# Optimization experiments

Hardware: AMD Instinct MI355X
Metric: run time of the kernel (lower is better)

The kernel has to match this reference:

```python
import jax, jax.numpy as jnp
import numpy as np
from jax.scipy.linalg import expm

S = 64          # alphabet size (codons)
M = 8           # number of models, prod(model_shape)
N_LEAVES = 32   # leaves of the balanced binary tree
N_EDGES = 62    # nodes 0..62, every non-root node has one parent edge (edge id == child node id)
B = 1024        # batch (alignment columns)
# per-level ranges of child-node ids; node 32+j has children (2j, 2j+1), etc.
LEVELS = [(0, 32), (32, 48), (48, 56), (56, 60), (60, 62)]


def inv_stereographic_projection(p):
    # maps R^{s-1} -> unit sphere S^{s-1}
    n2 = jnp.sum(p * p, axis=-1, keepdims=True)
    return jnp.concatenate([2.0 * p / (n2 + 1.0), (n2 - 1.0) / (n2 + 1.0)], axis=-1)


def generator(R, pi):
    # R: (M, s(s-1)/2) exchangeabilities, pi: (M, s) stationary distribution
    iu, ju = np.triu_indices(S, 1)
    A = jnp.zeros((M, S, S), R.dtype).at[:, iu, ju].set(R).at[:, ju, iu].set(R)
    Q = A * pi[:, None, :]                       # Q_ij = A_ij * pi_j (off-diagonal)
    row = jnp.sum(Q, axis=-1)                    # (M, S)
    return Q - jnp.eye(S, dtype=Q.dtype) * row[:, :, None]


def felsenstein(leave_configuration, R_inv, pi_inv, lengths):
    pi = inv_stereographic_projection(pi_inv) ** 2           # (M, S), rows sum to 1
    R = jnp.exp(R_inv)                                       # positive rates
    Q = generator(R, pi)                                     # (M, S, S)
    tQ = lengths[:, None, None, None] * Q[None]              # (E, M, S, S)
    P = jax.vmap(expm)(tQ.reshape(-1, S, S)).reshape(N_EDGES, M, S, S)
    # leaf alphas: tile leaf observations over the M models -> (n_leaves, B, M, S)
    prev = jnp.broadcast_to(
        leave_configuration.transpose(1, 0, 2)[:, :, None, :],
        (N_LEAVES, leave_configuration.shape[0], M, S))
    # level-synchronous pruning: messages up each parent edge, then product of the two children
    for a, b in LEVELS:
        msg = jnp.einsum('emcd,ebmd->ebmc', P[a:b], prev)    # per-edge transition
        prev = msg[0::2] * msg[1::2]                         # combine sibling pairs
    root = prev[0]                                           # (B, M, S)
    out = jnp.einsum('bms,ms->bm', root, pi)                 # P(data | model m)
    return out.reshape(out.shape[0], M)                      # (B, *model_shape)


def setup_inputs() -> dict:
    key = jax.random.key(0)
    k1, k2, k3, k4 = jax.random.split(key, 4)
    leave_configuration = jax.random.uniform(k1, (B, N_LEAVES, S), dtype=jnp.float32)
    tree_indices = jnp.zeros((B,), dtype=jnp.int32)          # single tree (F=1)
    R_inv = jax.random.uniform(k2, (M, S * (S - 1) // 2), dtype=jnp.float32,
                               minval=-1.0, maxval=1.0)
    pi_inv = jnp.full((M, S - 1), 1.0 / (np.sqrt(S) - 1.0), dtype=jnp.float32) \
        + 0.01 * jax.random.normal(k3, (M, S - 1), dtype=jnp.float32)
    lengths = jax.random.uniform(k4, (N_EDGES,), dtype=jnp.float32,
                                 minval=0.05, maxval=0.5)
    return {'leave_configuration': leave_configuration, 'R_inv': R_inv,
            'pi_inv': pi_inv, 'lengths': lengths, 'tree_indices': tree_indices}


def reference(leave_configuration, R_inv, pi_inv, lengths, tree_indices):
    # F=1: tf.dynamic_partition/gather_nd batch slicing is the identity, so
    # tree_indices is closed over / unused.
    return felsenstein(leave_configuration, R_inv, pi_inv, lengths)
```

## Files before the change

### kernel.cpp

```cpp
#include <hip/hip_runtime.h>

typedef unsigned short u16;
typedef unsigned int u32;
typedef __attribute__((ext_vector_type(8))) __bf16 bf16x8;
typedef __attribute__((ext_vector_type(4))) float f32x4;

constexpr size_t OFF_PI  = 0;
constexpr size_t OFF_PBH = 512;
constexpr size_t OFF_PBL = OFF_PBH + 1015808;

union FR { uint4 u; bf16x8 v; };

__device__ __forceinline__ void split_bf16(float x, u16& h, u16& l) {
  u32 b = __float_as_uint(x);
  u32 hb = (b + 0x7fffu + ((b >> 16) & 1u)) & 0xffff0000u;
  h = (u16)(hb >> 16);
  float r = x - __uint_as_float(hb);
  l = (u16)(__float_as_uint(r) >> 16);
}

__device__ __forceinline__ void split8(const f32x4 a, const f32x4 b,
                                       uint4& hi, uint4& lo) {
  u16 h[8], l[8];
  split_bf16(a.x, h[0], l[0]); split_bf16(a.y, h[1], l[1]);
  split_bf16(a.z, h[2], l[2]); split_bf16(a.w, h[3], l[3]);
  split_bf16(b.x, h[4], l[4]); split_bf16(b.y, h[5], l[5]);
  split_bf16(b.z, h[6], l[6]); split_bf16(b.w, h[7], l[7]);
  hi.x = h[0] | ((u32)h[1] << 16); hi.y = h[2] | ((u32)h[3] << 16);
  hi.z = h[4] | ((u32)h[5] << 16); hi.w = h[6] | ((u32)h[7] << 16);
  lo.x = l[0] | ((u32)l[1] << 16); lo.y = l[2] | ((u32)l[3] << 16);
  lo.z = l[4] | ((u32)l[5] << 16); lo.w = l[6] | ((u32)l[7] << 16);
}

__device__ __forceinline__ void mfma3(f32x4& a, const uint4 ah, const uint4 al,
                                      const uint4 bh, const uint4 bl) {
  FR Ah, Al, Bh, Bl;
  Ah.u = ah; Al.u = al; Bh.u = bh; Bl.u = bl;
  a = __builtin_amdgcn_mfma_f32_16x16x32_bf16(Ah.v, Bh.v, a, 0, 0, 0);
  a = __builtin_amdgcn_mfma_f32_16x16x32_bf16(Ah.v, Bl.v, a, 0, 0, 0);
  a = __builtin_amdgcn_mfma_f32_16x16x32_bf16(Al.v, Bh.v, a, 0, 0, 0);
}

__device__ __forceinline__ void xt_read2(const u32* b, int row, int chunk,
                                         uint4& hi, uint4& lo) {
  const int dw = (row << 5) + (((chunk + row) & 7) << 2);
  hi = *(const uint4*)&b[dw];
  lo = *(const uint4*)&b[2048 + dw];
}
__device__ __forceinline__ void xt_write4(u32* b, int row, int cp, int half,
                                          const f32x4 v) {
  u16 h[4], l[4];
  split_bf16(v.x, h[0], l[0]); split_bf16(v.y, h[1], l[1]);
  split_bf16(v.z, h[2], l[2]); split_bf16(v.w, h[3], l[3]);
  const int dw = (row << 5) + (((cp + row) & 7) << 2) + half * 2;
  uint2 hh, ll;
  hh.x = h[0] | ((u32)h[1] << 16); hh.y = h[2] | ((u32)h[3] << 16);
  ll.x = l[0] | ((u32)l[1] << 16); ll.y = l[2] | ((u32)l[3] << 16);
  *(uint2*)&b[dw] = hh;
  *(uint2*)&b[2048 + dw] = ll;
}

__global__ __launch_bounds__(512, 2) void k_pcomb(
    const float* __restrict__ R_inv, const float* __restrict__ pi_inv,
    const float* __restrict__ lengths, float* __restrict__ ws,
    u16* __restrict__ PBH, u16* __restrict__ PBL) {
  const int m = blockIdx.x & 7, prt = blockIdx.x >> 3;
  const int tid = threadIdx.x, lane = tid & 63, w = tid >> 6;
  const int ln = lane & 15, kq = lane >> 4;
  __shared__ float pis[64];
  __shared__ float n2s;
  __shared__ __align__(16) float Qs[64 * 68];
  __shared__ __align__(16) u32 PB[8][4096];

  if (tid < 64) {
    float p = (tid < 63) ? pi_inv[m * 63 + tid] : 0.f;
    float v = p * p;
    #pragma unroll
    for (int off = 32; off; off >>= 1) v += __shfl_down(v, off, 64);
    if (tid == 0) n2s = v;
  }
  __syncthreads();
  if (tid < 64) {
    const float den = n2s + 1.f;
    const float x = (tid < 63) ? 2.f * pi_inv[m * 63 + tid] / den
                               : (n2s - 1.f) / den;
    const float pv = x * x;
    pis[tid] = pv;
    if (prt == 0) ws[OFF_PI + (size_t)m * 64 + tid] = pv;
  }
  __syncthreads();
  for (int idx = tid; idx < 4096; idx += 512) {
    const int i = idx >> 6, j = idx & 63;
    float q = 0.f;
    if (i != j) {
      const int a = min(i, j), b = max(i, j);
      const int kk = a * (127 - a) / 2 + (b - a - 1);
      q = expf(R_inv[m * 2016 + kk]) * pis[j];
    }
    Qs[i * 68 + j] = q;
  }
  __syncthreads();
  if (tid < 64) {
    float s = 0.f;
    #pragma unroll 4
    for (int j4 = 0; j4 < 64; j4 += 4) {
      const f32x4 q = *(const f32x4*)&Qs[tid * 68 + j4];
      s += q.x + q.y + q.z + q.w;
    }
    Qs[tid * 68 + tid] = -s;
  }
  __syncthreads();
  float q[12][8];
  #pragma unroll
  for (int g = 0; g < 2; ++g) {
    const int vt = tid + 512 * g;
    const int ci0 = vt >> 4, cj0 = (vt & 15) * 4;
    #pragma unroll
    for (int r = 0; r < 4; ++r) q[0][g * 4 + r] = Qs[ci0 * 68 + cj0 + r];
  }
  {
    const int i = tid >> 3, c = tid & 7;
    const f32x4 a = *(const f32x4*)&Qs[i * 68 + c * 8];
    const f32x4 b = *(const f32x4*)&Qs[i * 68 + c * 8 + 4];
    uint4 h, l;
    split8(a, b, h, l);
    const int dw = (i << 5) + (((c + i) & 7) << 2);
    *(uint4*)&PB[0][dw] = h;
    *(uint4*)&PB[0][2048 + dw] = l;
    const int j = i;
    f32x4 ca, cb;
    ca.x = Qs[(c * 8 + 0) * 68 + j]; ca.y = Qs[(c * 8 + 1) * 68 + j];
    ca.z = Qs[(c * 8 + 2) * 68 + j]; ca.w = Qs[(c * 8 + 3) * 68 + j];
    cb.x = Qs[(c * 8 + 4) * 68 + j]; cb.y = Qs[(c * 8 + 5) * 68 + j];
    cb.z = Qs[(c * 8 + 6) * 68 + j]; cb.w = Qs[(c * 8 + 7) * 68 + j];
    split8(ca, cb, h, l);
    *(uint4*)&PB[4][dw] = h;
    *(uint4*)&PB[4][2048 + dw] = l;
  }
  __syncthreads();

  const f32x4 z = {0.f, 0.f, 0.f, 0.f};
  auto mm = [&](const u32* RX, const u32* CY, u32* dstC, u32* dstR) {
    #pragma unroll
    for (int tt = 0; tt < 2; ++tt) {
      const int T = w + tt * 8;
      const int ct = T >> 2, bt = T & 3;
      uint4 ah[2], al[2], bh[2], bl[2];
      #pragma unroll
      for (int kh = 0; kh < 2; ++kh) {
        xt_read2(RX, ct * 16 + ln, kh * 4 + kq, ah[kh], al[kh]);
        xt_read2(CY, bt * 16 + ln, kh * 4 + kq, bh[kh], bl[kh]);
      }
      f32x4 a = z;
      #pragma unroll
      for (int kh = 0; kh < 2; ++kh) mfma3(a, ah[kh], al[kh], bh[kh], bl[kh]);
      #pragma unroll
      for (int r = 0; r < 4; ++r)
        Qs[(ct * 16 + kq * 4 + r) * 64 + bt * 16 + ln] = a[r];
      if (dstC) xt_write4(dstC, bt * 16 + ln, 2 * ct + (kq >> 1), kq & 1, a);
      if (dstR) {
        uint4 ch[2], cl[2], dh[2], dl[2];
        #pragma unroll
        for (int kh = 0; kh < 2; ++kh) {
          xt_read2(CY, ct * 16 + ln, kh * 4 + kq, ch[kh], cl[kh]);
          xt_read2(RX, bt * 16 + ln, kh * 4 + kq, dh[kh], dl[kh]);
        }
        f32x4 a2 = z;
        #pragma unroll
        for (int kh = 0; kh < 2; ++kh) mfma3(a2, ch[kh], cl[kh], dh[kh], dl[kh]);
        xt_write4(dstR, bt * 16 + ln, 2 * ct + (kq >> 1), kq & 1, a2);
      }
    }
  };
  auto step = [&](const u32* RX, const u32* CY, int k, u32* dstC, u32* dstR) {
    mm(RX, CY, dstC, dstR);
    __syncthreads();
    #pragma unroll
    for (int g = 0; g < 2; ++g) {
      const int vt = tid + 512 * g;
      #pragma unroll
      for (int r = 0; r < 4; ++r) q[k - 1][g * 4 + r] = Qs[vt * 4 + r];
    }
    __syncthreads();
  };
  step(PB[0], PB[4], 2, PB[5], PB[1]);
  step(PB[1], PB[4], 3, PB[6], nullptr);
  step(PB[1], PB[5], 4, PB[7], PB[2]);
  step(PB[2], PB[4], 5, nullptr, nullptr);
  step(PB[2], PB[5], 6, nullptr, nullptr);
  step(PB[2], PB[6], 7, nullptr, nullptr);
  step(PB[2], PB[7], 8, nullptr, PB[3]);
  step(PB[3], PB[4], 9, nullptr, nullptr);
  step(PB[3], PB[5], 10, nullptr, nullptr);
  step(PB[3], PB[6], 11, nullptr, nullptr);
  step(PB[3], PB[7], 12, nullptr, nullptr);

  #pragma unroll
  for (int ei = 0; ei < 2; ++ei) {
    const int e = prt * 2 + ei;
    if (e >= 62) break;
    const float t = lengths[e];
    float av[8] = {0.f, 0.f, 0.f, 0.f, 0.f, 0.f, 0.f, 0.f};
    #pragma unroll
    for (int g = 0; g < 2; ++g) {
      const int vt = tid + 512 * g;
      const int dr = (vt >> 4) - ((vt & 15) * 4);
      if (dr >= 0 && dr < 4) av[g * 4 + dr] = 1.f;
    }
    float cf = 1.f;
    #pragma unroll
    for (int k = 1; k <= 12; ++k) {
      cf *= t / (float)k;
      #pragma unroll
      for (int r = 0; r < 8; ++r) av[r] = fmaf(cf, q[k - 1][r], av[r]);
    }
    #pragma unroll
    for (int g = 0; g < 2; ++g) {
      const int vt = tid + 512 * g;
      u16 h[4], l[4];
      split_bf16(av[g * 4 + 0], h[0], l[0]);
      split_bf16(av[g * 4 + 1], h[1], l[1]);
      split_bf16(av[g * 4 + 2], h[2], l[2]);
      split_bf16(av[g * 4 + 3], h[3], l[3]);
      const size_t base = (((size_t)e * 8 + m) << 12) + (size_t)vt * 4;
      ushort4 h4, l4;
      h4.x = h[0]; h4.y = h[1]; h4.z = h[2]; h4.w = h[3];
      l4.x = l[0]; l4.y = l[1]; l4.z = l[2]; l4.w = l[3];
      *(ushort4*)(PBH + base) = h4;
      *(ushort4*)(PBL + base) = l4;
    }
  }
}

__global__ __launch_bounds__(512, 2) void k_tree(
    const float* __restrict__ leaves, const u16* __restrict__ Phi,
    const u16* __restrict__ Plo, const float* __restrict__ ws,
    float* __restrict__ out) {
  const int m = blockIdx.x & 7, btile = blockIdx.x >> 3;
  const int tid = threadIdx.x, lane = tid & 63, w = tid >> 6;
  const int ln = lane & 15, kq = lane >> 4;
  __shared__ __align__(16) u32 slots[16 * 2048];
  __shared__ float psum[2][4][16];
  const f32x4 z = {0.f, 0.f, 0.f, 0.f};

  auto node_read = [&](int slot, int row, int kh, uint4& bh, uint4& bl) {
    const int jc = kh * 8 + kq * 2;
    const u32* b = &slots[slot * 2048 + row * 64];
    const uint4 A = *(const uint4*)&b[((jc + row) & 15) << 2];
    const uint4 B = *(const uint4*)&b[((jc + 1 + row) & 15) << 2];
    bh.x = A.x; bh.y = A.y; bh.z = B.x; bh.w = B.y;
    bl.x = A.z; bl.y = A.w; bl.z = B.z; bl.w = B.w;
  };
  auto node_write = [&](int slot, int row, int jc, const f32x4 v) {
    u16 h[4], l[4];
    split_bf16(v.x, h[0], l[0]); split_bf16(v.y, h[1], l[1]);
    split_bf16(v.z, h[2], l[2]); split_bf16(v.w, h[3], l[3]);
    uint4 pk;
    pk.x = h[0] | ((u32)h[1] << 16); pk.y = h[2] | ((u32)h[3] << 16);
    pk.z = l[0] | ((u32)l[1] << 16); pk.w = l[2] | ((u32)l[3] << 16);
    *(uint4*)&slots[slot * 2048 + row * 64 + (((jc + row) & 15) << 2)] = pk;
  };

  auto do_pair = [&](int eb, int p, int s0, int s1, int outSlot, int bt0,
                     int nbt, int ct0, int nct, bool leaf, f32x4* rootout) {
    uint4 bfh[2][2][2], bfl[2][2][2];
    #pragma unroll
    for (int s = 0; s < 2; ++s)
      #pragma unroll
      for (int bi = 0; bi < 2; ++bi) {
        if (bi >= nbt) continue;
        const int row = (bt0 + bi) * 16 + ln;
        #pragma unroll
        for (int kh = 0; kh < 2; ++kh) {
          if (leaf) {
            const float* g = leaves + (size_t)(btile * 32 + row) * 2048 +
                             (size_t)(eb + 2 * p + s) * 64 + kh * 32 + kq * 8;
            const f32x4 xa = *(const f32x4*)g;
            const f32x4 xb = *(const f32x4*)(g + 4);
            split8(xa, xb, bfh[s][bi][kh], bfl[s][bi][kh]);
          } else {
            node_read(s ? s1 : s0, row, kh, bfh[s][bi][kh], bfl[s][bi][kh]);
          }
        }
      }
    uint4 ph[2][4][2], pl[2][4][2];
    #pragma unroll
    for (int s = 0; s < 2; ++s) {
      const size_t pb = ((size_t)(eb + 2 * p + s) * 8 + m) << 12;
      #pragma unroll
      for (int ci = 0; ci < 4; ++ci) {
        if (ci >= nct) continue;
        #pragma unroll
        for (int kh = 0; kh < 2; ++kh) {
          const size_t off =
              pb + (size_t)((ct0 + ci) * 16 + ln) * 64 + kh * 32 + kq * 8;
          ph[s][ci][kh] = *(const uint4*)(Phi + off);
          pl[s][ci][kh] = *(const uint4*)(Plo + off);
        }
      }
    }
    f32x4 a0[4][2];
    #pragma unroll
    for (int ci = 0; ci < 4; ++ci) {
      if (ci >= nct) continue;
      #pragma unroll
      for (int bi = 0; bi < 2; ++bi) {
        if (bi >= nbt) continue;
        f32x4 a = z;
        #pragma unroll
        for (int kh = 0; kh < 2; ++kh)
          mfma3(a, ph[0][ci][kh], pl[0][ci][kh], bfh[0][bi][kh], bfl[0][bi][kh]);
        a0[ci][bi] = a;
      }
    }
    #pragma unroll
    for (int ci = 0; ci < 4; ++ci) {
      if (ci >= nct) continue;
      #pragma unroll
      for (int bi = 0; bi < 2; ++bi) {
        if (bi >= nbt) continue;
        f32x4 a = z;
        #pragma unroll
        for (int kh = 0; kh < 2; ++kh)
          mfma3(a, ph[1][ci][kh], pl[1][ci][kh], bfh[1][bi][kh], bfl[1][bi][kh]);
        const f32x4 pr = a0[ci][bi] * a;
        if (rootout)
          *rootout = pr;
        else
          node_write(outSlot, (bt0 + bi) * 16 + ln, (ct0 + ci) * 4 + kq, pr);
      }
    }
  };

  do_pair(0, w, -1, -1, w, 0, 2, 0, 4, true, nullptr);
  do_pair(0, w + 8, -1, -1, w + 8, 0, 2, 0, 4, true, nullptr);
  __syncthreads();
  do_pair(32, w, 2 * w, 2 * w + 1, 2 * w, 0, 2, 0, 4, false, nullptr);
  __syncthreads();
  {
    const int j = w >> 1, bi = w & 1;
    do_pair(48, j, 4 * j, 4 * j + 2, 4 * j, bi, 1, 0, 4, false, nullptr);
  }
  __syncthreads();
  {
    const int j = w >> 2, bi = w & 1, ch = (w >> 1) & 1;
    do_pair(56, j, 8 * j, 8 * j + 4, 8 * j + 1, bi, 1, ch * 2, 2, false,
            nullptr);
  }
  __syncthreads();
  {
    f32x4 pr = z;
    do_pair(60, 0, 1, 9, -1, w & 1, 1, w >> 1, 1, false, &pr);
    const f32x4 piv =
        *(const f32x4*)&ws[OFF_PI + (size_t)m * 64 + (w >> 1) * 16 + kq * 4];
    float v = pr.x * piv.x + pr.y * piv.y + pr.z * piv.z + pr.w * piv.w;
    v += __shfl_xor(v, 16, 64);
    v += __shfl_xor(v, 32, 64);
    if (lane < 16) psum[w & 1][w >> 1][lane] = v;
  }
  __syncthreads();
  if (tid < 32) {
    const int bi = tid >> 4, bb = tid & 15;
    out[(size_t)(btile * 32 + tid) * 8 + m] =
        psum[bi][0][bb] + psum[bi][1][bb] + psum[bi][2][bb] + psum[bi][3][bb];
  }
}

extern "C" void kernel_launch(void* const* d_in, const int* in_sizes, int n_in,
                              void* d_out, int out_size, void* d_ws, size_t ws_size,
                              hipStream_t stream) {
  const float* leaves  = (const float*)d_in[0];
  const float* R_inv   = (const float*)d_in[1];
  const float* pi_inv  = (const float*)d_in[2];
  const float* lengths = (const float*)d_in[3];
  float* out = (float*)d_out;
  float* ws  = (float*)d_ws;

  u16* PBH = (u16*)(ws + OFF_PBH);
  u16* PBL = (u16*)(ws + OFF_PBL);

  hipLaunchKernelGGL(k_pcomb, dim3(256), dim3(512), 0, stream, R_inv, pi_inv,
                     lengths, ws, PBH, PBL);
  hipLaunchKernelGGL(k_tree, dim3(256), dim3(512), 0, stream, leaves, PBH, PBL,
                     ws, out);
}
```

Measured before the change: 122.5 us.

## Fuse P-matrix build and tree pruning into one kernel with a grid barrier

Merges the transition-matrix build kernel and the tree-pruning kernel into a single launch of 256 blocks. An atomic-counter grid-wide barrier separates the two phases, and both phases share one shared-memory buffer. The aim is to remove the second launch and the inter-kernel gap. The barrier assumes all 256 blocks are co-resident, otherwise it deadlocks, and the 2-blocks-per-CU launch bound was dropped.

```diff
diff --git a/kernel.cpp b/kernel.cpp
--- a/kernel.cpp
+++ b/kernel.cpp
@@ -10,6 +10,8 @@
 constexpr size_t OFF_PBL = OFF_PBH + 1015808;
 
 union FR { uint4 u; bf16x8 v; };
+
+__device__ unsigned g_bar = 0;
 
 __device__ __forceinline__ void split_bf16(float x, u16& h, u16& l) {
   u32 b = __float_as_uint(x);
@@ -60,309 +62,328 @@
   *(uint2*)&b[2048 + dw] = ll;
 }
 
-__global__ __launch_bounds__(512, 2) void k_pcomb(
-    const float* __restrict__ R_inv, const float* __restrict__ pi_inv,
-    const float* __restrict__ lengths, float* __restrict__ ws,
-    u16* __restrict__ PBH, u16* __restrict__ PBL) {
-  const int m = blockIdx.x & 7, prt = blockIdx.x >> 3;
+__global__ __launch_bounds__(512) void k_fused(
+    const float* __restrict__ leaves, const float* __restrict__ R_inv,
+    const float* __restrict__ pi_inv, const float* __restrict__ lengths,
+    float* __restrict__ ws, u16* __restrict__ PBH, u16* __restrict__ PBL,
+    float* __restrict__ out) {
+  const int m = blockIdx.x & 7;
   const int tid = threadIdx.x, lane = tid & 63, w = tid >> 6;
   const int ln = lane & 15, kq = lane >> 4;
-  __shared__ float pis[64];
-  __shared__ float n2s;
-  __shared__ __align__(16) float Qs[64 * 68];
-  __shared__ __align__(16) u32 PB[8][4096];
-
-  if (tid < 64) {
-    float p = (tid < 63) ? pi_inv[m * 63 + tid] : 0.f;
-    float v = p * p;
-    #pragma unroll
-    for (int off = 32; off; off >>= 1) v += __shfl_down(v, off, 64);
-    if (tid == 0) n2s = v;
-  }
-  __syncthreads();
-  if (tid < 64) {
-    const float den = n2s + 1.f;
-    const float x = (tid < 63) ? 2.f * pi_inv[m * 63 + tid] / den
-                               : (n2s - 1.f) / den;
-    const float pv = x * x;
-    pis[tid] = pv;
-    if (prt == 0) ws[OFF_PI + (size_t)m * 64 + tid] = pv;
-  }
-  __syncthreads();
-  for (int idx = tid; idx < 4096; idx += 512) {
-    const int i = idx >> 6, j = idx & 63;
-    float q = 0.f;
-    if (i != j) {
-      const int a = min(i, j), b = max(i, j);
-      const int kk = a * (127 - a) / 2 + (b - a - 1);
-      q = expf(R_inv[m * 2016 + kk]) * pis[j];
-    }
-    Qs[i * 68 + j] = q;
-  }
-  __syncthreads();
-  if (tid < 64) {
-    float s = 0.f;
-    #pragma unroll 4
-    for (int j4 = 0; j4 < 64; j4 += 4) {
-      const f32x4 q = *(const f32x4*)&Qs[tid * 68 + j4];
-      s += q.x + q.y + q.z + q.w;
-    }
-    Qs[tid * 68 + tid] = -s;
-  }
-  __syncthreads();
-  float q[12][8];
-  #pragma unroll
-  for (int g = 0; g < 2; ++g) {
-    const int vt = tid + 512 * g;
-    const int ci0 = vt >> 4, cj0 = (vt & 15) * 4;
-    #pragma unroll
-    for (int r = 0; r < 4; ++r) q[0][g * 4 + r] = Qs[ci0 * 68 + cj0 + r];
-  }
+  __shared__ __align__(16) u32 smem[37200];
+  const f32x4 z = {0.f, 0.f, 0.f, 0.f};
+
   {
-    const int i = tid >> 3, c = tid & 7;
-    const f32x4 a = *(const f32x4*)&Qs[i * 68 + c * 8];
-    const f32x4 b = *(const f32x4*)&Qs[i * 68 + c * 8 + 4];
-    uint4 h, l;
-    split8(a, b, h, l);
-    const int dw = (i << 5) + (((c + i) & 7) << 2);
-    *(uint4*)&PB[0][dw] = h;
-    *(uint4*)&PB[0][2048 + dw] = l;
-    const int j = i;
-    f32x4 ca, cb;
-    ca.x = Qs[(c * 8 + 0) * 68 + j]; ca.y = Qs[(c * 8 + 1) * 68 + j];
-    ca.z = Qs[(c * 8 + 2) * 68 + j]; ca.w = Qs[(c * 8 + 3) * 68 + j];
-    cb.x = Qs[(c * 8 + 4) * 68 + j]; cb.y = Qs[(c * 8 + 5) * 68 + j];
-    cb.z = Qs[(c * 8 + 6) * 68 + j]; cb.w = Qs[(c * 8 + 7) * 68 + j];
-    split8(ca, cb, h, l);
-    *(uint4*)&PB[4][dw] = h;
-    *(uint4*)&PB[4][2048 + dw] = l;
-  }
-  __syncthreads();
-
-  const f32x4 z = {0.f, 0.f, 0.f, 0.f};
-  auto mm = [&](const u32* RX, const u32* CY, u32* dstC, u32* dstR) {
-    #pragma unroll
-    for (int tt = 0; tt < 2; ++tt) {
-      const int T = w + tt * 8;
-      const int ct = T >> 2, bt = T & 3;
-      uint4 ah[2], al[2], bh[2], bl[2];
-      #pragma unroll
-      for (int kh = 0; kh < 2; ++kh) {
-        xt_read2(RX, ct * 16 + ln, kh * 4 + kq, ah[kh], al[kh]);
-        xt_read2(CY, bt * 16 + ln, kh * 4 + kq, bh[kh], bl[kh]);
-      }
-      f32x4 a = z;
-      #pragma unroll
-      for (int kh = 0; kh < 2; ++kh) mfma3(a, ah[kh], al[kh], bh[kh], bl[kh]);
-      #pragma unroll
-      for (int r = 0; r < 4; ++r)
-        Qs[(ct * 16 + kq * 4 + r) * 64 + bt * 16 + ln] = a[r];
-      if (dstC) xt_write4(dstC, bt * 16 + ln, 2 * ct + (kq >> 1), kq & 1, a);
-      if (dstR) {
-        uint4 ch[2], cl[2], dh[2], dl[2];
-        #pragma unroll
-        for (int kh = 0; kh < 2; ++kh) {
-          xt_read2(CY, ct * 16 + ln, kh * 4 + kq, ch[kh], cl[kh]);
-          xt_read2(RX, bt * 16 + ln, kh * 4 + kq, dh[kh], dl[kh]);
-        }
-        f32x4 a2 = z;
-        #pragma unroll
-        for (int kh = 0; kh < 2; ++kh) mfma3(a2, ch[kh], cl[kh], dh[kh], dl[kh]);
-        xt_write4(dstR, bt * 16 + ln, 2 * ct + (kq >> 1), kq & 1, a2);
-      }
-    }
-  };
-  auto step = [&](const u32* RX, const u32* CY, int k, u32* dstC, u32* dstR) {
-    mm(RX, CY, dstC, dstR);
-    __syncthreads();
+    const int prt = blockIdx.x >> 3;
+    float* pis = (float*)smem;
+    float* Qs  = (float*)&smem[80];
+    u32* PB    = &smem[4432];
+
+    if (tid < 64) {
+      float p = (tid < 63) ? pi_inv[m * 63 + tid] : 0.f;
+      float v = p * p;
+      #pragma unroll
+      for (int off = 32; off; off >>= 1) v += __shfl_down(v, off, 64);
+      if (tid == 0) ((float*)smem)[64] = v;
+    }
+    __syncthreads();
+    if (tid < 64) {
+      const float n2v = ((float*)smem)[64];
+      const float den = n2v + 1.f;
+      const float x = (tid < 63) ? 2.f * pi_inv[m * 63 + tid] / den
+                                 : (n2v - 1.f) / den;
+      const float pv = x * x;
+      pis[tid] = pv;
+      if (prt == 0) ws[OFF_PI + (size_t)m * 64 + tid] = pv;
+    }
+    __syncthreads();
+    for (int idx = tid; idx < 4096; idx += 512) {
+      const int i = idx >> 6, j = idx & 63;
+      float q = 0.f;
+      if (i != j) {
+        const int a = min(i, j), b = max(i, j);
+        const int kk = a * (127 - a) / 2 + (b - a - 1);
+        q = expf(R_inv[m * 2016 + kk]) * pis[j];
+      }
+      Qs[i * 68 + j] = q;
+    }
+    __syncthreads();
+    if (tid < 64) {
+      float s = 0.f;
+      #pragma unroll 4
+      for (int j4 = 0; j4 < 64; j4 += 4) {
+        const f32x4 q = *(const f32x4*)&Qs[tid * 68 + j4];
+        s += q.x + q.y + q.z + q.w;
+      }
+      Qs[tid * 68 + tid] = -s;
+    }
+    __syncthreads();
+    float q[12][8];
     #pragma unroll
     for (int g = 0; g < 2; ++g) {
       const int vt = tid + 512 * g;
-      #pragma unroll
-      for (int r = 0; r < 4; ++r) q[k - 1][g * 4 + r] = Qs[vt * 4 + r];
-    }
-    __syncthreads();
-  };
-  step(PB[0], PB[4], 2, PB[5], PB[1]);
-  step(PB[1], PB[4], 3, PB[6], nullptr);
-  step(PB[1], PB[5], 4, PB[7], PB[2]);
-  step(PB[2], PB[4], 5, nullptr, nullptr);
-  step(PB[2], PB[5], 6, nullptr, nullptr);
-  step(PB[2], PB[6], 7, nullptr, nullptr);
-  step(PB[2], PB[7], 8, nullptr, PB[3]);
-  step(PB[3], PB[4], 9, nullptr, nullptr);
-  step(PB[3], PB[5], 10, nullptr, nullptr);
-  step(PB[3], PB[6], 11, nullptr, nullptr);
-  step(PB[3], PB[7], 12, nullptr, nullptr);
-
-  #pragma unroll
-  for (int ei = 0; ei < 2; ++ei) {
-    const int e = prt * 2 + ei;
-    if (e >= 62) break;
-    const float t = lengths[e];
-    float av[8] = {0.f, 0.f, 0.f, 0.f, 0.f, 0.f, 0.f, 0.f};
+      const int ci0 = vt >> 4, cj0 = (vt & 15) * 4;
+      #pragma unroll
+      for (int r = 0; r < 4; ++r) q[0][g * 4 + r] = Qs[ci0 * 68 + cj0 + r];
+    }
+    {
+      const int i = tid >> 3, c = tid & 7;
+      const f32x4 a = *(const f32x4*)&Qs[i * 68 + c * 8];
+      const f32x4 b = *(const f32x4*)&Qs[i * 68 + c * 8 + 4];
+      uint4 h, l;
+      split8(a, b, h, l);
+      const int dw = (i << 5) + (((c + i) & 7) << 2);
+      *(uint4*)&PB[dw] = h;
+      *(uint4*)&PB[2048 + dw] = l;
+      const int j = i;
+      f32x4 ca, cb;
+      ca.x = Qs[(c * 8 + 0) * 68 + j]; ca.y = Qs[(c * 8 + 1) * 68 + j];
+      ca.z = Qs[(c * 8 + 2) * 68 + j]; ca.w = Qs[(c * 8 + 3) * 68 + j];
+      cb.x = Qs[(c * 8 + 4) * 68 + j]; cb.y = Qs[(c * 8 + 5) * 68 + j];
+      cb.z = Qs[(c * 8 + 6) * 68 + j]; cb.w = Qs[(c * 8 + 7) * 68 + j];
+      split8(ca, cb, h, l);
+      *(uint4*)&PB[4 * 4096 + dw] = h;
+      *(uint4*)&PB[4 * 4096 + 2048 + dw] = l;
+    }
+    __syncthreads();
+
+    auto mm = [&](const u32* RX, const u32* CY, u32* dstC, u32* dstR) {
+      #pragma unroll
+      for (int tt = 0; tt < 2; ++tt) {
+        const int T = w + tt * 8;
+        const int ct = T >> 2, bt = T & 3;
+        uint4 ah[2], al[2], bh[2], bl[2];
+        #pragma unroll
+        for (int kh = 0; kh < 2; ++kh) {
+          xt_read2(RX, ct * 16 + ln, kh * 4 + kq, ah[kh], al[kh]);
+          xt_read2(CY, bt * 16 + ln, kh * 4 + kq, bh[kh], bl[kh]);
+        }
+        f32x4 a = z;
+        #pragma unroll
+        for (int kh = 0; kh < 2; ++kh) mfma3(a, ah[kh], al[kh], bh[kh], bl[kh]);
+        #pragma unroll
+        for (int r = 0; r < 4; ++r)
+          Qs[(ct * 16 + kq * 4 + r) * 64 + bt * 16 + ln] = a[r];
+        if (dstC) xt_write4(dstC, bt * 16 + ln, 2 * ct + (kq >> 1), kq & 1, a);
+        if (dstR) {
+          uint4 ch[2], cl[2], dh[2], dl[2];
+          #pragma unroll
+          for (int kh = 0; kh < 2; ++kh) {
+            xt_read2(CY, ct * 16 + ln, kh * 4 + kq, ch[kh], cl[kh]);
+            xt_read2(RX, bt * 16 + ln, kh * 4 + kq, dh[kh], dl[kh]);
+          }
+          f32x4 a2 = z;
+          #pragma unroll
+          for (int kh = 0; kh < 2; ++kh)
+            mfma3(a2, ch[kh], cl[kh], dh[kh], dl[kh]);
+          xt_write4(dstR, bt * 16 + ln, 2 * ct + (kq >> 1), kq & 1, a2);
+        }
+      }
+    };
+    auto step = [&](const u32* RX, const u32* CY, int k, u32* dstC, u32* dstR) {
+      mm(RX, CY, dstC, dstR);
+      __syncthreads();
+      #pragma unroll
+      for (int g = 0; g < 2; ++g) {
+        const int vt = tid + 512 * g;
+        #pragma unroll
+        for (int r = 0; r < 4; ++r) q[k - 1][g * 4 + r] = Qs[vt * 4 + r];
+      }
+      __syncthreads();
+    };
+    u32* P0 = PB;            u32* P1 = PB + 1 * 4096;
+    u32* P2 = PB + 2 * 4096; u32* P3 = PB + 3 * 4096;
+    u32* P4 = PB + 4 * 4096; u32* P5 = PB + 5 * 4096;
+    u32* P6 = PB + 6 * 4096; u32* P7 = PB + 7 * 4096;
+    step(P0, P4, 2, P5, P1);
+    step(P1, P4, 3, P6, nullptr);
+    step(P1, P5, 4, P7, P2);
+    step(P2, P4, 5, nullptr, nullptr);
+    step(P2, P5, 6, nullptr, nullptr);
+    step(P2, P6, 7, nullptr, nullptr);
+    step(P2, P7, 8, nullptr, P3);
+    step(P3, P4, 9, nullptr, nullptr);
+    step(P3, P5, 10, nullptr, nullptr);
+    step(P3, P6, 11, nullptr, nullptr);
+    step(P3, P7, 12, nullptr, nullptr);
+
     #pragma unroll
-    for (int g = 0; g < 2; ++g) {
-      const int vt = tid + 512 * g;
-      const int dr = (vt >> 4) - ((vt & 15) * 4);
-      if (dr >= 0 && dr < 4) av[g * 4 + dr] = 1.f;
-    }
-    float cf = 1.f;
-    #pragma unroll
-    for (int k = 1; k <= 12; ++k) {
-      cf *= t / (float)k;
-      #pragma unroll
-      for (int r = 0; r < 8; ++r) av[r] = fmaf(cf, q[k - 1][r], av[r]);
-    }
-    #pragma unroll
-    for (int g = 0; g < 2; ++g) {
-      const int vt = tid + 512 * g;
+    for (int ei = 0; ei < 2; ++ei) {
+      const int e = prt * 2 + ei;
+      if (e >= 62) break;
+      const float t = lengths[e];
+      float av[8] = {0.f, 0.f, 0.f, 0.f, 0.f, 0.f, 0.f, 0.f};
+      #pragma unroll
+      for (int g = 0; g < 2; ++g) {
+        const int vt = tid + 512 * g;
+        const int dr = (vt >> 4) - ((vt & 15) * 4);
+        if (dr >= 0 && dr < 4) av[g * 4 + dr] = 1.f;
+      }
+      float cf = 1.f;
+      #pragma unroll
+      for (int k = 1; k <= 12; ++k) {
+        cf *= t / (float)k;
+        #pragma unroll
+        for (int r = 0; r < 8; ++r) av[r] = fmaf(cf, q[k - 1][r], av[r]);
+      }
+      #pragma unroll
+      for (int g = 0; g < 2; ++g) {
+        const int vt = tid + 512 * g;
+        u16 h[4], l[4];
+        split_bf16(av[g * 4 + 0], h[0], l[0]);
+        split_bf16(av[g * 4 + 1], h[1], l[1]);
+        split_bf16(av[g * 4 + 2], h[2], l[2]);
+        split_bf16(av[g * 4 + 3], h[3], l[3]);
+        const size_t base = (((size_t)e * 8 + m) << 12) + (size_t)vt * 4;
+        ushort4 h4, l4;
+        h4.x = h[0]; h4.y = h[1]; h4.z = h[2]; h4.w = h[3];
+        l4.x = l[0]; l4.y = l[1]; l4.z = l[2]; l4.w = l[3];
+        *(ushort4*)(PBH + base) = h4;
+        *(ushort4*)(PBL + base) = l4;
+      }
+    }
+  }
+
+  __syncthreads();
+  if (tid == 0) {
+    __threadfence();
+    const unsigned old = atomicAdd(&g_bar, 1u);
+    const unsigned target = (old & ~255u) + 256u;
+    while (__hip_atomic_load(&g_bar, __ATOMIC_ACQUIRE,
+                             __HIP_MEMORY_SCOPE_AGENT) < target)
+      __builtin_amdgcn_s_sleep(2);
+  }
+  __syncthreads();
+
+  {
+    const int btile = blockIdx.x >> 3;
+    u32* slots = smem;
+    float* psum = (float*)&smem[32768];
+
+    auto node_read = [&](int slot, int row, int kh, uint4& bh, uint4& bl) {
+      const int jc = kh * 8 + kq * 2;
+      const u32* b = &slots[slot * 2048 + row * 64];
+      const uint4 A = *(const uint4*)&b[((jc + row) & 15) << 2];
+      const uint4 B = *(const uint4*)&b[((jc + 1 + row) & 15) << 2];
+      bh.x = A.x; bh.y = A.y; bh.z = B.x; bh.w = B.y;
+      bl.x = A.z; bl.y = A.w; bl.z = B.z; bl.w = B.w;
+    };
+    auto node_write = [&](int slot, int row, int jc, const f32x4 v) {
       u16 h[4], l[4];
-      split_bf16(av[g * 4 + 0], h[0], l[0]);
-      split_bf16(av[g * 4 + 1], h[1], l[1]);
-      split_bf16(av[g * 4 + 2], h[2], l[2]);
-      split_bf16(av[g * 4 + 3], h[3], l[3]);
-      const size_t base = (((size_t)e * 8 + m) << 12) + (size_t)vt * 4;
-      ushort4 h4, l4;
-      h4.x = h[0]; h4.y = h[1]; h4.z = h[2]; h4.w = h[3];
-      l4.x = l[0]; l4.y = l[1]; l4.z = l[2]; l4.w = l[3];
-      *(ushort4*)(PBH + base) = h4;
-      *(ushort4*)(PBL + base) = l4;
-    }
-  }
-}
-
-__global__ __launch_bounds__(512, 2) void k_tree(
-    const float* __restrict__ leaves, const u16* __restrict__ Phi,
-    const u16* __restrict__ Plo, const float* __restrict__ ws,
-    float* __restrict__ out) {
-  const int m = blockIdx.x & 7, btile = blockIdx.x >> 3;
-  const int tid = threadIdx.x, lane = tid & 63, w = tid >> 6;
-  const int ln = lane & 15, kq = lane >> 4;
-  __shared__ __align__(16) u32 slots[16 * 2048];
-  __shared__ float psum[2][4][16];
-  const f32x4 z = {0.f, 0.f, 0.f, 0.f};
-
-  auto node_read = [&](int slot, int row, int kh, uint4& bh, uint4& bl) {
-    const int jc = kh * 8 + kq * 2;
-    const u32* b = &slots[slot * 2048 + row * 64];
-    const uint4 A = *(const uint4*)&b[((jc + row) & 15) << 2];
-    const uint4 B = *(const uint4*)&b[((jc + 1 + row) & 15) << 2];
-    bh.x = A.x; bh.y = A.y; bh.z = B.x; bh.w = B.y;
-    bl.x = A.z; bl.y = A.w; bl.z = B.z; bl.w = B.w;
-  };
-  auto node_write = [&](int slot, int row, int jc, const f32x4 v) {
-    u16 h[4], l[4];
-    split_bf16(v.x, h[0], l[0]); split_bf16(v.y, h[1], l[1]);
-    split_bf16(v.z, h[2], l[2]); split_bf16(v.w, h[3], l[3]);
-    uint4 pk;
-    pk.x = h[0] | ((u32)h[1] << 16); pk.y = h[2] | ((u32)h[3] << 16);
-    pk.z = l[0] | ((u32)l[1] << 16); pk.w = l[2] | ((u32)l[3] << 16);
-    *(uint4*)&slots[slot * 2048 + row * 64 + (((jc + row) & 15) << 2)] = pk;
-  };
-
-  auto do_pair = [&](int eb, int p, int s0, int s1, int outSlot, int bt0,
-                     int nbt, int ct0, int nct, bool leaf, f32x4* rootout) {
-    uint4 bfh[2][2][2], bfl[2][2][2];
-    #pragma unroll
-    for (int s = 0; s < 2; ++s)
-      #pragma unroll
-      for (int bi = 0; bi < 2; ++bi) {
-        if (bi >= nbt) continue;
-        const int row = (bt0 + bi) * 16 + ln;
-        #pragma unroll
-        for (int kh = 0; kh < 2; ++kh) {
-          if (leaf) {
-            const float* g = leaves + (size_t)(btile * 32 + row) * 2048 +
-                             (size_t)(eb + 2 * p + s) * 64 + kh * 32 + kq * 8;
-            const f32x4 xa = *(const f32x4*)g;
-            const f32x4 xb = *(const f32x4*)(g + 4);
-            split8(xa, xb, bfh[s][bi][kh], bfl[s][bi][kh]);
-          } else {
-            node_read(s ? s1 : s0, row, kh, bfh[s][bi][kh], bfl[s][bi][kh]);
+      split_bf16(v.x, h[0], l[0]); split_bf16(v.y, h[1], l[1]);
+      split_bf16(v.z, h[2], l[2]); split_bf16(v.w, h[3], l[3]);
+      uint4 pk;
+      pk.x = h[0] | ((u32)h[1] << 16); pk.y = h[2] | ((u32)h[3] << 16);
+      pk.z = l[0] | ((u32)l[1] << 16); pk.w = l[2] | ((u32)l[3] << 16);
+      *(uint4*)&slots[slot * 2048 + row * 64 + (((jc + row) & 15) << 2)] = pk;
+    };
+
+    auto do_pair = [&](int eb, int p, int s0, int s1, int outSlot, int bt0,
+                       int nbt, int ct0, int nct, bool leaf, f32x4* rootout) {
+      uint4 bfh[2][2][2], bfl[2][2][2];
+      #pragma unroll
+      for (int s = 0; s < 2; ++s)
+        #pragma unroll
+        for (int bi = 0; bi < 2; ++bi) {
+          if (bi >= nbt) continue;
+          const int row = (bt0 + bi) * 16 + ln;
+          #pragma unroll
+          for (int kh = 0; kh < 2; ++kh) {
+            if (leaf) {
+              const float* g = leaves + (size_t)(btile * 32 + row) * 2048 +
+                               (size_t)(eb + 2 * p + s) * 64 + kh * 32 + kq * 8;
+              const f32x4 xa = *(const f32x4*)g;
+              const f32x4 xb = *(const f32x4*)(g + 4);
+              split8(xa, xb, bfh[s][bi][kh], bfl[s][bi][kh]);
+            } else {
+              node_read(s ? s1 : s0, row, kh, bfh[s][bi][kh], bfl[s][bi][kh]);
+            }
           }
         }
-      }
-    uint4 ph[2][4][2], pl[2][4][2];
-    #pragma unroll
-    for (int s = 0; s < 2; ++s) {
-      const size_t pb = ((size_t)(eb + 2 * p + s) * 8 + m) << 12;
+      uint4 ph[2][4][2], pl[2][4][2];
+      #pragma unroll
+      for (int s = 0; s < 2; ++s) {
+        const size_t pb = ((size_t)(eb + 2 * p + s) * 8 + m) << 12;
+        #pragma unroll
+        for (int ci = 0; ci < 4; ++ci) {
+          if (ci >= nct) continue;
+          #pragma unroll
+          for (int kh = 0; kh < 2; ++kh) {
+            const size_t off =
+                pb + (size_t)((ct0 + ci) * 16 + ln) * 64 + kh * 32 + kq * 8;
+            ph[s][ci][kh] = *(const uint4*)(PBH + off);
+            pl[s][ci][kh] = *(const uint4*)(PBL + off);
+          }
+        }
+      }
+      f32x4 a0[4][2];
       #pragma unroll
       for (int ci = 0; ci < 4; ++ci) {
         if (ci >= nct) continue;
         #pragma unroll
-        for (int kh = 0; kh < 2; ++kh) {
-          const size_t off =
-              pb + (size_t)((ct0 + ci) * 16 + ln) * 64 + kh * 32 + kq * 8;
-          ph[s][ci][kh] = *(const uint4*)(Phi + off);
-          pl[s][ci][kh] = *(const uint4*)(Plo + off);
-        }
-      }
-    }
-    f32x4 a0[4][2];
-    #pragma unroll
-    for (int ci = 0; ci < 4; ++ci) {
-      if (ci >= nct) continue;
-      #pragma unroll
-      for (int bi = 0; bi < 2; ++bi) {
-        if (bi >= nbt) continue;
-        f32x4 a = z;
-        #pragma unroll
-        for (int kh = 0; kh < 2; ++kh)
-          mfma3(a, ph[0][ci][kh], pl[0][ci][kh], bfh[0][bi][kh], bfl[0][bi][kh]);
-        a0[ci][bi] = a;
-      }
-    }
-    #pragma unroll
-    for (int ci = 0; ci < 4; ++ci) {
-      if (ci >= nct) continue;
-      #pragma unroll
-      for (int bi = 0; bi < 2; ++bi) {
-        if (bi >= nbt) continue;
-        f32x4 a = z;
-        #pragma unroll
-        for (int kh = 0; kh < 2; ++kh)
-          mfma3(a, ph[1][ci][kh], pl[1][ci][kh], bfh[1][bi][kh], bfl[1][bi][kh]);
-        const f32x4 pr = a0[ci][bi] * a;
-        if (rootout)
-          *rootout = pr;
-        else
-          node_write(outSlot, (bt0 + bi) * 16 + ln, (ct0 + ci) * 4 + kq, pr);
-      }
-    }
-  };
-
-  do_pair(0, w, -1, -1, w, 0, 2, 0, 4, true, nullptr);
-  do_pair(0, w + 8, -1, -1, w + 8, 0, 2, 0, 4, true, nullptr);
-  __syncthreads();
-  do_pair(32, w, 2 * w, 2 * w + 1, 2 * w, 0, 2, 0, 4, false, nullptr);
-  __syncthreads();
-  {
-    const int j = w >> 1, bi = w & 1;
-    do_pair(48, j, 4 * j, 4 * j + 2, 4 * j, bi, 1, 0, 4, false, nullptr);
-  }
-  __syncthreads();
-  {
-    const int j = w >> 2, bi = w & 1, ch = (w >> 1) & 1;
-    do_pair(56, j, 8 * j, 8 * j + 4, 8 * j + 1, bi, 1, ch * 2, 2, false,
-            nullptr);
-  }
-  __syncthreads();
-  {
-    f32x4 pr = z;
-    do_pair(60, 0, 1, 9, -1, w & 1, 1, w >> 1, 1, false, &pr);
-    const f32x4 piv =
-        *(const f32x4*)&ws[OFF_PI + (size_t)m * 64 + (w >> 1) * 16 + kq * 4];
-    float v = pr.x * piv.x + pr.y * piv.y + pr.z * piv.z + pr.w * piv.w;
-    v += __shfl_xor(v, 16, 64);
-    v += __shfl_xor(v, 32, 64);
-    if (lane < 16) psum[w & 1][w >> 1][lane] = v;
-  }
-  __syncthreads();
-  if (tid < 32) {
-    const int bi = tid >> 4, bb = tid & 15;
-    out[(size_t)(btile * 32 + tid) * 8 + m] =
-        psum[bi][0][bb] + psum[bi][1][bb] + psum[bi][2][bb] + psum[bi][3][bb];
+        for (int bi = 0; bi < 2; ++bi) {
+          if (bi >= nbt) continue;
+          f32x4 a = z;
+          #pragma unroll
+          for (int kh = 0; kh < 2; ++kh)
+            mfma3(a, ph[0][ci][kh], pl[0][ci][kh], bfh[0][bi][kh],
+                  bfl[0][bi][kh]);
+          a0[ci][bi] = a;
+        }
+      }
+      #pragma unroll
+      for (int ci = 0; ci < 4; ++ci) {
+        if (ci >= nct) continue;
+        #pragma unroll
+        for (int bi = 0; bi < 2; ++bi) {
+          if (bi >= nbt) continue;
+          f32x4 a = z;
+          #pragma unroll
+          for (int kh = 0; kh < 2; ++kh)
+            mfma3(a, ph[1][ci][kh], pl[1][ci][kh], bfh[1][bi][kh],
+                  bfl[1][bi][kh]);
+          const f32x4 pr = a0[ci][bi] * a;
+          if (rootout)
+            *rootout = pr;
+          else
+            node_write(outSlot, (bt0 + bi) * 16 + ln, (ct0 + ci) * 4 + kq, pr);
+        }
+      }
+    };
+
+    do_pair(0, w, -1, -1, w, 0, 2, 0, 4, true, nullptr);
+    do_pair(0, w + 8, -1, -1, w + 8, 0, 2, 0, 4, true, nullptr);
+    __syncthreads();
+    do_pair(32, w, 2 * w, 2 * w + 1, 2 * w, 0, 2, 0, 4, false, nullptr);
+    __syncthreads();
+    {
+      const int j = w >> 1, bi = w & 1;
+      do_pair(48, j, 4 * j, 4 * j + 2, 4 * j, bi, 1, 0, 4, false, nullptr);
+    }
+    __syncthreads();
+    {
+      const int j = w >> 2, bi = w & 1, ch = (w >> 1) & 1;
+      do_pair(56, j, 8 * j, 8 * j + 4, 8 * j + 1, bi, 1, ch * 2, 2, false,
+              nullptr);
+    }
+    __syncthreads();
+    {
+      f32x4 pr = z;
+      do_pair(60, 0, 1, 9, -1, w & 1, 1, w >> 1, 1, false, &pr);
+      const f32x4 piv =
+          *(const f32x4*)&ws[OFF_PI + (size_t)m * 64 + (w >> 1) * 16 + kq * 4];
+      float v = pr.x * piv.x + pr.y * piv.y + pr.z * piv.z + pr.w * piv.w;
+      v += __shfl_xor(v, 16, 64);
+      v += __shfl_xor(v, 32, 64);
+      if (lane < 16) psum[((w & 1) * 4 + (w >> 1)) * 16 + lane] = v;
+    }
+    __syncthreads();
+    if (tid < 32) {
+      const int bi = tid >> 4, bb = tid & 15;
+      out[(size_t)(btile * 32 + tid) * 8 + m] =
+          psum[(bi * 4 + 0) * 16 + bb] + psum[(bi * 4 + 1) * 16 + bb] +
+          psum[(bi * 4 + 2) * 16 + bb] + psum[(bi * 4 + 3) * 16 + bb];
+    }
   }
 }
 
@@ -379,8 +400,6 @@
   u16* PBH = (u16*)(ws + OFF_PBH);
   u16* PBL = (u16*)(ws + OFF_PBL);
 
-  hipLaunchKernelGGL(k_pcomb, dim3(256), dim3(512), 0, stream, R_inv, pi_inv,
-                     lengths, ws, PBH, PBL);
-  hipLaunchKernelGGL(k_tree, dim3(256), dim3(512), 0, stream, leaves, PBH, PBL,
-                     ws, out);
-}
+  hipLaunchKernelGGL(k_fused, dim3(256), dim3(512), 0, stream, leaves, R_inv,
+                     pi_inv, lengths, ws, PBH, PBL, out);
+}
```

After: 145.0 us. +18.4%, slower.

## Keep Q power tiles in MFMA register layout and batch independent power products

Applied to the files above, without the earlier changes.

The Taylor-series powers of Q are now kept in registers in the MFMA accumulator layout, so they no longer pass through shared memory with a barrier pair after each power. Independent products (Q^2..Q^12 from the shared PB buffers) are grouped into four dependency stages, which cuts eleven two-barrier steps down to three barriers. In exchange, the final P stores become scattered 2-byte writes to global memory instead of ushort4 vector stores, and more accumulators stay live at once.

```diff
diff --git a/kernel.cpp b/kernel.cpp
--- a/kernel.cpp
+++ b/kernel.cpp
@@ -110,13 +110,14 @@
     Qs[tid * 68 + tid] = -s;
   }
   __syncthreads();
-  float q[12][8];
-  #pragma unroll
-  for (int g = 0; g < 2; ++g) {
-    const int vt = tid + 512 * g;
-    const int ci0 = vt >> 4, cj0 = (vt & 15) * 4;
-    #pragma unroll
-    for (int r = 0; r < 4; ++r) q[0][g * 4 + r] = Qs[ci0 * 68 + cj0 + r];
+
+  float q[12][2][4];
+  #pragma unroll
+  for (int tt = 0; tt < 2; ++tt) {
+    const int T = w + tt * 8, ct = T >> 2, bt = T & 3;
+    #pragma unroll
+    for (int r = 0; r < 4; ++r)
+      q[0][tt][r] = Qs[(ct * 16 + kq * 4 + r) * 68 + bt * 16 + ln];
   }
   {
     const int i = tid >> 3, c = tid & 7;
@@ -140,94 +141,117 @@
   __syncthreads();
 
   const f32x4 z = {0.f, 0.f, 0.f, 0.f};
-  auto mm = [&](const u32* RX, const u32* CY, u32* dstC, u32* dstR) {
-    #pragma unroll
-    for (int tt = 0; tt < 2; ++tt) {
-      const int T = w + tt * 8;
-      const int ct = T >> 2, bt = T & 3;
-      uint4 ah[2], al[2], bh[2], bl[2];
-      #pragma unroll
-      for (int kh = 0; kh < 2; ++kh) {
-        xt_read2(RX, ct * 16 + ln, kh * 4 + kq, ah[kh], al[kh]);
-        xt_read2(CY, bt * 16 + ln, kh * 4 + kq, bh[kh], bl[kh]);
-      }
-      f32x4 a = z;
-      #pragma unroll
-      for (int kh = 0; kh < 2; ++kh) mfma3(a, ah[kh], al[kh], bh[kh], bl[kh]);
-      #pragma unroll
-      for (int r = 0; r < 4; ++r)
-        Qs[(ct * 16 + kq * 4 + r) * 64 + bt * 16 + ln] = a[r];
-      if (dstC) xt_write4(dstC, bt * 16 + ln, 2 * ct + (kq >> 1), kq & 1, a);
-      if (dstR) {
-        uint4 ch[2], cl[2], dh[2], dl[2];
-        #pragma unroll
-        for (int kh = 0; kh < 2; ++kh) {
-          xt_read2(CY, ct * 16 + ln, kh * 4 + kq, ch[kh], cl[kh]);
-          xt_read2(RX, bt * 16 + ln, kh * 4 + kq, dh[kh], dl[kh]);
-        }
-        f32x4 a2 = z;
-        #pragma unroll
-        for (int kh = 0; kh < 2; ++kh) mfma3(a2, ch[kh], cl[kh], dh[kh], dl[kh]);
-        xt_write4(dstR, bt * 16 + ln, 2 * ct + (kq >> 1), kq & 1, a2);
-      }
-    }
-  };
-  auto step = [&](const u32* RX, const u32* CY, int k, u32* dstC, u32* dstR) {
-    mm(RX, CY, dstC, dstR);
-    __syncthreads();
-    #pragma unroll
-    for (int g = 0; g < 2; ++g) {
-      const int vt = tid + 512 * g;
-      #pragma unroll
-      for (int r = 0; r < 4; ++r) q[k - 1][g * 4 + r] = Qs[vt * 4 + r];
-    }
-    __syncthreads();
-  };
-  step(PB[0], PB[4], 2, PB[5], PB[1]);
-  step(PB[1], PB[4], 3, PB[6], nullptr);
-  step(PB[1], PB[5], 4, PB[7], PB[2]);
-  step(PB[2], PB[4], 5, nullptr, nullptr);
-  step(PB[2], PB[5], 6, nullptr, nullptr);
-  step(PB[2], PB[6], 7, nullptr, nullptr);
-  step(PB[2], PB[7], 8, nullptr, PB[3]);
-  step(PB[3], PB[4], 9, nullptr, nullptr);
-  step(PB[3], PB[5], 10, nullptr, nullptr);
-  step(PB[3], PB[6], 11, nullptr, nullptr);
-  step(PB[3], PB[7], 12, nullptr, nullptr);
+  auto tileP = [&](const u32* RX, const u32* CY, int T) -> f32x4 {
+    const int ct = T >> 2, bt = T & 3;
+    uint4 ah[2], al[2], bh[2], bl[2];
+    #pragma unroll
+    for (int kh = 0; kh < 2; ++kh) {
+      xt_read2(RX, ct * 16 + ln, kh * 4 + kq, ah[kh], al[kh]);
+      xt_read2(CY, bt * 16 + ln, kh * 4 + kq, bh[kh], bl[kh]);
+    }
+    f32x4 a = z;
+    #pragma unroll
+    for (int kh = 0; kh < 2; ++kh) mfma3(a, ah[kh], al[kh], bh[kh], bl[kh]);
+    return a;
+  };
+  auto tileT = [&](const u32* RX, const u32* CY, int T) -> f32x4 {
+    const int ct = T >> 2, bt = T & 3;
+    uint4 ah[2], al[2], bh[2], bl[2];
+    #pragma unroll
+    for (int kh = 0; kh < 2; ++kh) {
+      xt_read2(CY, ct * 16 + ln, kh * 4 + kq, ah[kh], al[kh]);
+      xt_read2(RX, bt * 16 + ln, kh * 4 + kq, bh[kh], bl[kh]);
+    }
+    f32x4 a = z;
+    #pragma unroll
+    for (int kh = 0; kh < 2; ++kh) mfma3(a, ah[kh], al[kh], bh[kh], bl[kh]);
+    return a;
+  };
+  auto wbuf = [&](u32* dst, int T, const f32x4 a) {
+    const int ct = T >> 2, bt = T & 3;
+    xt_write4(dst, bt * 16 + ln, 2 * ct + (kq >> 1), kq & 1, a);
+  };
+
+  #pragma unroll
+  for (int tt = 0; tt < 2; ++tt) {
+    const int T = w + tt * 8;
+    const f32x4 a = tileP(PB[0], PB[4], T);
+    #pragma unroll
+    for (int r = 0; r < 4; ++r) q[1][tt][r] = a[r];
+    wbuf(PB[5], T, a);
+    wbuf(PB[1], T, tileT(PB[0], PB[4], T));
+  }
+  __syncthreads();
+  #pragma unroll
+  for (int tt = 0; tt < 2; ++tt) {
+    const int T = w + tt * 8;
+    const f32x4 a3 = tileP(PB[1], PB[4], T);
+    const f32x4 a4 = tileP(PB[1], PB[5], T);
+    #pragma unroll
+    for (int r = 0; r < 4; ++r) { q[2][tt][r] = a3[r]; q[3][tt][r] = a4[r]; }
+    wbuf(PB[6], T, a3);
+    wbuf(PB[7], T, a4);
+    wbuf(PB[2], T, tileT(PB[1], PB[5], T));
+  }
+  __syncthreads();
+  #pragma unroll
+  for (int tt = 0; tt < 2; ++tt) {
+    const int T = w + tt * 8;
+    const f32x4 a5 = tileP(PB[2], PB[4], T);
+    const f32x4 a6 = tileP(PB[2], PB[5], T);
+    const f32x4 a7 = tileP(PB[2], PB[6], T);
+    const f32x4 a8 = tileP(PB[2], PB[7], T);
+    #pragma unroll
+    for (int r = 0; r < 4; ++r) {
+      q[4][tt][r] = a5[r]; q[5][tt][r] = a6[r];
+      q[6][tt][r] = a7[r]; q[7][tt][r] = a8[r];
+    }
+    wbuf(PB[3], T, tileT(PB[2], PB[7], T));
+  }
+  __syncthreads();
+  #pragma unroll
+  for (int tt = 0; tt < 2; ++tt) {
+    const int T = w + tt * 8;
+    const f32x4 a9  = tileP(PB[3], PB[4], T);
+    const f32x4 a10 = tileP(PB[3], PB[5], T);
+    const f32x4 a11 = tileP(PB[3], PB[6], T);
+    const f32x4 a12 = tileP(PB[3], PB[7], T);
+    #pragma unroll
+    for (int r = 0; r < 4; ++r) {
+      q[8][tt][r] = a9[r];  q[9][tt][r] = a10[r];
+      q[10][tt][r] = a11[r]; q[11][tt][r] = a12[r];
+    }
+  }
 
   #pragma unroll
   for (int ei = 0; ei < 2; ++ei) {
     const int e = prt * 2 + ei;
     if (e >= 62) break;
     const float t = lengths[e];
-    float av[8] = {0.f, 0.f, 0.f, 0.f, 0.f, 0.f, 0.f, 0.f};
-    #pragma unroll
-    for (int g = 0; g < 2; ++g) {
-      const int vt = tid + 512 * g;
-      const int dr = (vt >> 4) - ((vt & 15) * 4);
-      if (dr >= 0 && dr < 4) av[g * 4 + dr] = 1.f;
-    }
-    float cf = 1.f;
-    #pragma unroll
-    for (int k = 1; k <= 12; ++k) {
-      cf *= t / (float)k;
-      #pragma unroll
-      for (int r = 0; r < 8; ++r) av[r] = fmaf(cf, q[k - 1][r], av[r]);
-    }
-    #pragma unroll
-    for (int g = 0; g < 2; ++g) {
-      const int vt = tid + 512 * g;
-      u16 h[4], l[4];
-      split_bf16(av[g * 4 + 0], h[0], l[0]);
-      split_bf16(av[g * 4 + 1], h[1], l[1]);
-      split_bf16(av[g * 4 + 2], h[2], l[2]);
-      split_bf16(av[g * 4 + 3], h[3], l[3]);
-      const size_t base = (((size_t)e * 8 + m) << 12) + (size_t)vt * 4;
-      ushort4 h4, l4;
-      h4.x = h[0]; h4.y = h[1]; h4.z = h[2]; h4.w = h[3];
-      l4.x = l[0]; l4.y = l[1]; l4.z = l[2]; l4.w = l[3];
-      *(ushort4*)(PBH + base) = h4;
-      *(ushort4*)(PBL + base) = l4;
+    const size_t base = ((size_t)e * 8 + m) << 12;
+    #pragma unroll
+    for (int tt = 0; tt < 2; ++tt) {
+      const int T = w + tt * 8, ct = T >> 2, bt = T & 3;
+      float av[4];
+      #pragma unroll
+      for (int r = 0; r < 4; ++r)
+        av[r] = (ct == bt && ln == kq * 4 + r) ? 1.f : 0.f;
+      float cf = 1.f;
+      #pragma unroll
+      for (int k = 1; k <= 12; ++k) {
+        cf *= t / (float)k;
+        #pragma unroll
+        for (int r = 0; r < 4; ++r) av[r] = fmaf(cf, q[k - 1][tt][r], av[r]);
+      }
+      #pragma unroll
+      for (int r = 0; r < 4; ++r) {
+        u16 h, l;
+        split_bf16(av[r], h, l);
+        const size_t off =
+            base + (size_t)(ct * 16 + kq * 4 + r) * 64 + bt * 16 + ln;
+        PBH[off] = h;
+        PBL[off] = l;
+      }
     }
   }
 }
```

New measurement: 119.8 us (median of 3 runs). 1.02x faster.
